# Performance work log

Measured on AMD Instinct MI355X. Metric: run time of the kernel, lower is better.

The kernel has to match this reference:

```python
import jax, jax.numpy as jnp
import numpy as np
import math

B, S, MEM, D, H = 2, 2048, 512, 1024, 16
DH = D // H  # 64


def setup_inputs() -> dict:
    key = jax.random.key(0)
    ks = jax.random.split(key, 12)
    s = 1.0 / math.sqrt(D)
    return {
        "x": jax.random.normal(ks[0], (B, S, D), jnp.float32),
        "mems": jax.random.normal(ks[1], (B, MEM, D), jnp.float32),
        "freqs_cis": jax.random.normal(ks[2], (S, 32), jnp.float32),
        "mask": jax.random.randint(ks[3], (B, MEM + S), 0, 2, jnp.int32),
        "Wq": jax.random.normal(ks[4], (D, D), jnp.float32) * s,
        "bq": jnp.zeros((D,), jnp.float32),
        "Wk": jax.random.normal(ks[5], (D, D), jnp.float32) * s,
        "bk": jnp.zeros((D,), jnp.float32),
        "Wv": jax.random.normal(ks[6], (D, D), jnp.float32) * s,
        "bv": jnp.zeros((D,), jnp.float32),
        "Wo": jax.random.normal(ks[7], (D, D), jnp.float32) * s,
        "bo": jnp.zeros((D,), jnp.float32),
    }


def _split_heads(t):
    # [B, T, D] -> [B, H, T, DH]
    b, t_, _ = t.shape
    return t.reshape(b, t_, H, DH).transpose(0, 2, 1, 3)


def reference(x, mems, freqs_cis, mask, Wq, bq, Wk, bk, Wv, bv, Wo, bo):
    # mems prepended along sequence for K/V (torch: c = cat([mems, x], 1))
    c = jnp.concatenate([mems, x], axis=1)  # [B, MEM+S, D]
    Q = _split_heads(x @ Wq.T + bq)          # [B, H, S, DH]
    K = _split_heads(c @ Wk.T + bk)          # [B, H, Skv, DH]
    V = _split_heads(c @ Wv.T + bv)          # [B, H, Skv, DH]

    scores = jnp.einsum("bhqd,bhkd->bhqk", Q, K) / math.sqrt(DH)
    m = mask.astype(jnp.float32)             # [B, Skv]
    scores = scores - 1e6 * (1.0 - m[:, None, None, :])
    attn = jax.nn.softmax(scores, axis=-1)   # dropout omitted (eval mode)
    out = jnp.einsum("bhqk,bhkd->bhqd", attn, V)  # [B, H, S, DH]
    out = out.transpose(0, 2, 1, 3).reshape(B, S, D)
    return out @ Wo.T + bo
```

## Files before the change

### kernel.cpp

```cpp
#include <hip/hip_runtime.h>
#include <math.h>

#define NB   2
#define SQ   2048
#define SMEM 512
#define SKVN 2560
#define ND   1024
#define NH   16
#define DHN  64
#define NBH  32

typedef unsigned short u16;
typedef short bf16x8 __attribute__((ext_vector_type(8)));
typedef float f32x4 __attribute__((ext_vector_type(4)));
typedef u16 u16x4 __attribute__((ext_vector_type(4)));
typedef u16 u16x8 __attribute__((ext_vector_type(8)));

#define CSC   0.1803368801111204f

__device__ __forceinline__ u16 f2bf(float f) {
    unsigned u = __float_as_uint(f);
    u += 0x7FFFu + ((u >> 16) & 1u);
    return (u16)(u >> 16);
}

__device__ __forceinline__ float bf2f(u16 v) {
    return __uint_as_float(((unsigned)v) << 16);
}

__device__ __forceinline__ void async16(u16* lds, const u16* g) {
    __builtin_amdgcn_global_load_lds(
        (const __attribute__((address_space(1))) void*)g,
        (__attribute__((address_space(3))) void*)lds, 16, 0, 0);
}

__device__ __forceinline__ unsigned lds_off(const void* p) {
    return (unsigned)(uintptr_t)(const __attribute__((address_space(3))) void*)p;
}

__device__ __forceinline__ u16x4 tr_read(unsigned a) {
    u16x4 d;
    asm volatile("ds_read_b64_tr_b16 %0, %1" : "=v"(d) : "v"(a) : "memory");
    return d;
}

__device__ __forceinline__ unsigned cvtpk(float lo, float hi) {
    unsigned r;
    asm("v_cvt_pk_bf16_f32 %0, %1, %2" : "=v"(r) : "v"(lo), "v"(hi));
    return r;
}

__device__ __forceinline__ float exp2r(float x) {
    float r;
    asm("v_exp_f32 %0, %1" : "=v"(r) : "v"(x));
    return r;
}

union PKU { unsigned u[2]; u16x4 v; };
union U8  { struct { u16x4 lo, hi; } p; bf16x8 v; };

__global__ __launch_bounds__(256)
void cvt_all(const float* __restrict__ x, const float* __restrict__ mems,
             const float* __restrict__ W0, const float* __restrict__ W1,
             const float* __restrict__ W2, const float* __restrict__ W3,
             u16* __restrict__ xb, u16* __restrict__ memb,
             u16* __restrict__ d0, u16* __restrict__ d1,
             u16* __restrict__ d2, u16* __restrict__ d3,
             const int* __restrict__ mask, u16* __restrict__ mb16)
{
    const int bid = blockIdx.x;
    if (bid >= 4608) {
        const int i = (bid - 4608) * 256 + threadIdx.x;
        if (i < NB * SKVN)
            mb16[i] = mask[i] ? (u16)0 : f2bf(1.0e6f * CSC);
        return;
    }
    size_t i = ((size_t)bid * 256 + threadIdx.x) * 8;
    const float* s; u16* d;
    if (i < 4194304) { s = x; d = xb; }
    else if (i < 5242880) { s = mems; d = memb; i -= 4194304; }
    else {
        size_t off = i - 5242880;
        const int wi = (int)(off >> 20);
        i = off & 1048575;
        switch (wi) {
            case 0:  s = W0; d = d0; break;
            case 1:  s = W1; d = d1; break;
            case 2:  s = W2; d = d2; break;
            default: s = W3; d = d3; break;
        }
    }
    float4 a = *(const float4*)(s + i);
    float4 b = *(const float4*)(s + i + 4);
    u16x8 o;
    o[0]=f2bf(a.x); o[1]=f2bf(a.y); o[2]=f2bf(a.z); o[3]=f2bf(a.w);
    o[4]=f2bf(b.x); o[5]=f2bf(b.y); o[6]=f2bf(b.z); o[7]=f2bf(b.w);
    *(u16x8*)(d + i) = o;
}

__device__ __forceinline__ const u16* arow_ptr(const u16* x, const u16* mems,
                                               int grow, int T, int memLen) {
    int b = grow >= T ? 1 : 0;
    int t = grow - b * T;
    if (memLen > 0 && t < memLen)
        return mems + ((size_t)(b * memLen + t)) * ND;
    return x + ((size_t)(b * (T - memLen) + (t - memLen))) * ND;
}

__device__ __forceinline__
void gemm_body(const u16* __restrict__ x, const u16* __restrict__ mems,
               const u16* __restrict__ W, const float* __restrict__ bias,
               void* __restrict__ out, int T, int memLen, int mode,
               int bx, int by, u16* As0, u16* As1, u16* Bs0, u16* Bs1)
{
    u16* As[2] = {As0, As1};
    u16* Bs[2] = {Bs0, Bs1};

    const int tid  = threadIdx.x;
    const int wave = tid >> 6, lane = tid & 63;
    const int lg = lane >> 4, li = lane & 15;
    const int wr = (wave >> 1) * 64, wc = (wave & 1) * 64;
    const int row0 = bx * 128, col0 = by * 128;

    const int srow = lane >> 2;
    const int sslot = lane & 3;

    f32x4 acc[4][4];
    const f32x4 zf = {0.f, 0.f, 0.f, 0.f};
#pragma unroll
    for (int m = 0; m < 4; ++m)
#pragma unroll
        for (int n = 0; n < 4; ++n) acc[m][n] = zf;

    auto stage = [&](int c, int kt) {
        const int k0 = kt * 32;
#pragma unroll
        for (int ch = wave; ch < 8; ch += 4) {
            const int r = ch * 16 + srow;
            const int gs = sslot ^ ((r ^ (r >> 2)) & 3);
            async16(&As[c][ch * 512],
                    arow_ptr(x, mems, row0 + r, T, memLen) + k0 + gs * 8);
        }
#pragma unroll
        for (int ch = wave; ch < 8; ch += 4) {
            const int r = ch * 16 + srow;
            const int gs = sslot ^ ((r ^ (r >> 2)) & 3);
            async16(&Bs[c][ch * 512],
                    W + (size_t)(col0 + r) * ND + k0 + gs * 8);
        }
    };

    stage(0, 0);
    __builtin_amdgcn_sched_barrier(0);
    stage(1, 1);
    __builtin_amdgcn_sched_barrier(0);

    int cur = 0;
    for (int kt = 0; kt < 32; ++kt) {
        if (kt == 31) asm volatile("s_waitcnt vmcnt(0)" ::: "memory");
        else          asm volatile("s_waitcnt vmcnt(4)" ::: "memory");
        __builtin_amdgcn_s_barrier();
        __builtin_amdgcn_sched_barrier(0);

        bf16x8 af[4], bfr[4];
#pragma unroll
        for (int m = 0; m < 4; ++m) {
            const int r = wr + m * 16 + li;
            af[m] = *(const bf16x8*)&As[cur][r * 32 + ((lg ^ ((r ^ (r >> 2)) & 3)) << 3)];
        }
#pragma unroll
        for (int n = 0; n < 4; ++n) {
            const int r = wc + n * 16 + li;
            bfr[n] = *(const bf16x8*)&Bs[cur][r * 32 + ((lg ^ ((r ^ (r >> 2)) & 3)) << 3)];
        }
#pragma unroll
        for (int m = 0; m < 4; ++m)
#pragma unroll
            for (int n = 0; n < 4; ++n)
                acc[m][n] = __builtin_amdgcn_mfma_f32_16x16x32_bf16(
                                af[m], bfr[n], acc[m][n], 0, 0, 0);

        asm volatile("s_waitcnt lgkmcnt(0)" ::: "memory");
        __builtin_amdgcn_s_barrier();
        __builtin_amdgcn_sched_barrier(0);

        if (kt + 2 < 32) stage(cur, kt + 2);
        cur ^= 1;
    }

#pragma unroll
    for (int n = 0; n < 4; ++n) {
        const int col = col0 + wc + n * 16 + li;
        const float bv = bias[col];
#pragma unroll
        for (int m = 0; m < 4; ++m) {
            const int rbase = row0 + wr + m * 16 + 4 * lg;
            if (mode == 1) {
                u16* o = (u16*)out;
                const int h = col >> 6, dh = col & 63;
#pragma unroll
                for (int r = 0; r < 4; ++r) {
                    const int grow = rbase + r;
                    const int b = grow >= T ? 1 : 0;
                    const int t = grow - b * T;
                    o[(((size_t)b * NH + h) * T + t) * DHN + dh] =
                        f2bf(acc[m][n][r] + bv);
                }
            } else {
                u16* o = (u16*)out;
                const int h = col >> 6, dh = col & 63;
                const int b = rbase >= T ? 1 : 0;
                const int t = rbase - b * T;
                u16x4 pk;
                pk[0] = f2bf(acc[m][n][0] + bv);
                pk[1] = f2bf(acc[m][n][1] + bv);
                pk[2] = f2bf(acc[m][n][2] + bv);
                pk[3] = f2bf(acc[m][n][3] + bv);
                *(u16x4*)&o[(((size_t)b * NH + h) * DHN + dh) * (size_t)T + t] = pk;
            }
        }
    }
}

__global__ __launch_bounds__(256)
void gemm_qkv(const u16* __restrict__ xb, const u16* __restrict__ memb,
              const u16* __restrict__ Wq, const float* __restrict__ bq, u16* Qb,
              const u16* __restrict__ Wk, const float* __restrict__ bk, u16* Kb,
              const u16* __restrict__ Wv, const float* __restrict__ bv, u16* Vtb)
{
    __shared__ u16 As[2][128 * 32];
    __shared__ u16 Bs[2][128 * 32];
    const int id = (blockIdx.x & 7) * 112 + (blockIdx.x >> 3);
    if (id < 256) {
        gemm_body(xb, nullptr, Wq, bq, Qb, SQ, 0, 1, id & 31, id >> 5,
                  As[0], As[1], Bs[0], Bs[1]);
    } else if (id < 576) {
        const int t = id - 256;
        gemm_body(xb, memb, Wk, bk, Kb, SKVN, SMEM, 1, t % 40, t / 40,
                  As[0], As[1], Bs[0], Bs[1]);
    } else {
        const int t = id - 576;
        gemm_body(xb, memb, Wv, bv, Vtb, SKVN, SMEM, 2, t % 40, t / 40,
                  As[0], As[1], Bs[0], Bs[1]);
    }
}

__global__ __launch_bounds__(256)
void gemm_o(const u16* __restrict__ x, const u16* __restrict__ W,
            const float* __restrict__ bias, float* __restrict__ out)
{
    __shared__ u16 As[2][64 * 32];
    __shared__ u16 Bs[2][128 * 32];

    const int tid  = threadIdx.x;
    const int wave = tid >> 6, lane = tid & 63;
    const int lg = lane >> 4, li = lane & 15;
    const int wr = (wave >> 1) * 32, wc = (wave & 1) * 64;

    const int id = (blockIdx.x & 7) * 64 + (blockIdx.x >> 3);
    const int row0 = (id >> 3) * 64, col0 = (id & 7) * 128;

    const int srow = lane >> 2;
    const int sslot = lane & 3;

    f32x4 acc[2][4];
    const f32x4 zf = {0.f, 0.f, 0.f, 0.f};
#pragma unroll
    for (int m = 0; m < 2; ++m)
#pragma unroll
        for (int n = 0; n < 4; ++n) acc[m][n] = zf;

    auto stage = [&](int c, int kt) {
        const int k0 = kt * 32;
        {
            const int r = wave * 16 + srow;
            const int gs = sslot ^ ((r ^ (r >> 2)) & 3);
            async16(&As[c][wave * 512],
                    x + (size_t)(row0 + r) * ND + k0 + gs * 8);
        }
#pragma unroll
        for (int ch = wave; ch < 8; ch += 4) {
            const int r = ch * 16 + srow;
            const int gs = sslot ^ ((r ^ (r >> 2)) & 3);
            async16(&Bs[c][ch * 512],
                    W + (size_t)(col0 + r) * ND + k0 + gs * 8);
        }
    };

    stage(0, 0);
    __builtin_amdgcn_sched_barrier(0);
    stage(1, 1);
    __builtin_amdgcn_sched_barrier(0);

    int cur = 0;
    for (int kt = 0; kt < 32; ++kt) {
        if (kt == 31) asm volatile("s_waitcnt vmcnt(0)" ::: "memory");
        else          asm volatile("s_waitcnt vmcnt(3)" ::: "memory");
        __builtin_amdgcn_s_barrier();
        __builtin_amdgcn_sched_barrier(0);

        bf16x8 af[2], bfr[4];
#pragma unroll
        for (int m = 0; m < 2; ++m) {
            const int r = wr + m * 16 + li;
            af[m] = *(const bf16x8*)&As[cur][r * 32 + ((lg ^ ((r ^ (r >> 2)) & 3)) << 3)];
        }
#pragma unroll
        for (int n = 0; n < 4; ++n) {
            const int r = wc + n * 16 + li;
            bfr[n] = *(const bf16x8*)&Bs[cur][r * 32 + ((lg ^ ((r ^ (r >> 2)) & 3)) << 3)];
        }
#pragma unroll
        for (int m = 0; m < 2; ++m)
#pragma unroll
            for (int n = 0; n < 4; ++n)
                acc[m][n] = __builtin_amdgcn_mfma_f32_16x16x32_bf16(
                                af[m], bfr[n], acc[m][n], 0, 0, 0);

        asm volatile("s_waitcnt lgkmcnt(0)" ::: "memory");
        __builtin_amdgcn_s_barrier();
        __builtin_amdgcn_sched_barrier(0);

        if (kt + 2 < 32) stage(cur, kt + 2);
        cur ^= 1;
    }

#pragma unroll
    for (int n = 0; n < 4; ++n) {
        const int col = col0 + wc + n * 16 + li;
        const float bv = bias[col];
#pragma unroll
        for (int m = 0; m < 2; ++m) {
            const int rbase = row0 + wr + m * 16 + 4 * lg;
#pragma unroll
            for (int r = 0; r < 4; ++r)
                out[(size_t)(rbase + r) * ND + col] = acc[m][n][r] + bv;
        }
    }
}

__global__ __launch_bounds__(512)
void attn_mfma(const u16* __restrict__ Qw, const u16* __restrict__ Kw,
               const u16* __restrict__ Vt, const u16* __restrict__ mb16,
               u16* __restrict__ AO)
{
    __shared__ u16 Ks[2][64 * 64];
    __shared__ u16 Vs[2][64 * 64];
    __shared__ u16 Ps[8][1024];
    __shared__ u16 Ms[SKVN];

    const int tid  = threadIdx.x;
    const int wave = tid >> 6, lane = tid & 63;
    const int lg = lane >> 4, li = lane & 15;

    const int wg = blockIdx.x;
    const int sw = (wg & 7) * 64 + (wg >> 3);
    const int bh = sw >> 4;
    const int q0 = (sw & 15) * 128;
    const int b = bh >> 4, h = bh & 15;

    const u16* Kg = Kw + (size_t)bh * SKVN * DHN;
    const u16* Vg = Vt + (size_t)bh * DHN * SKVN;
    const u16* m16row = mb16 + (size_t)b * SKVN;

    bf16x8 qA0, qA1;
    {
        const u16* Qp = Qw + ((size_t)bh * SQ + q0 + wave * 16 + li) * DHN;
        qA0 = *(const bf16x8*)(Qp + lg * 8);
        qA1 = *(const bf16x8*)(Qp + 32 + lg * 8);
    }

    for (int i = tid * 8; i < SKVN; i += 4096)
        *(u16x8*)&Ms[i] = *(const u16x8*)(m16row + i);

    U8 ou;
#pragma unroll
    for (int i = 0; i < 4; ++i) { ou.p.lo[i] = 0x3F80; ou.p.hi[i] = 0x3F80; }
    const bf16x8 onesb = ou.v;

    const int srow = lane >> 3, sslot = lane & 7;

    auto stage = [&](int c, int t) {
        const int kv0 = t * 64;
        const int r = wave * 8 + srow;
        async16(&Ks[c][wave * 512],
                Kg + (size_t)(kv0 + r) * DHN + ((sslot ^ (r & 7)) << 3));
        async16(&Vs[c][wave * 512],
                Vg + (size_t)r * SKVN + kv0 + ((sslot ^ (r & 7)) << 3));
    };

    f32x4 oA[4], laccA;
    const f32x4 zf = {0.f, 0.f, 0.f, 0.f};
#pragma unroll
    for (int n = 0; n < 4; ++n) oA[n] = zf;
    laccA = zf;

    u16* Pw = &Ps[wave][0];
    const unsigned paA = lds_off(Pw) + 256u * lg + 8u * li;

    __syncthreads();
    __builtin_amdgcn_sched_barrier(0);
    stage(0, 0);
    __builtin_amdgcn_sched_barrier(0);
    stage(1, 1);
    __builtin_amdgcn_sched_barrier(0);

    const int NT = SKVN / 64;
    int cur = 0;
    for (int t = 0; t < NT; ++t) {
        if (t == NT - 1) asm volatile("s_waitcnt vmcnt(0)" ::: "memory");
        else             asm volatile("s_waitcnt vmcnt(2)" ::: "memory");
        __builtin_amdgcn_s_barrier();
        __builtin_amdgcn_sched_barrier(0);

        float mbc[4];
#pragma unroll
        for (int n = 0; n < 4; ++n)
            mbc[n] = bf2f(Ms[t * 64 + n * 16 + li]);

        __builtin_amdgcn_s_setprio(1);
        f32x4 sA[4];
#pragma unroll
        for (int n = 0; n < 4; ++n) {
            const int r = n * 16 + li;
            bf16x8 kb0 = *(const bf16x8*)&Ks[cur][r * 64 + ((lg ^ (r & 7)) << 3)];
            bf16x8 kb1 = *(const bf16x8*)&Ks[cur][r * 64 + (((4 + lg) ^ (r & 7)) << 3)];
            f32x4 z = zf;
            z     = __builtin_amdgcn_mfma_f32_16x16x32_bf16(qA0, kb0, z, 0, 0, 0);
            sA[n] = __builtin_amdgcn_mfma_f32_16x16x32_bf16(qA1, kb1, z, 0, 0, 0);
        }
        __builtin_amdgcn_s_setprio(0);

#pragma unroll
        for (int n = 0; n < 4; ++n) {
            const float mb = mbc[n];
            const int pw = (n * 16 + li) * 16 + lg * 4;
            PKU ua;
            ua.u[0] = cvtpk(exp2r(fmaf(sA[n][0], CSC, -mb)),
                            exp2r(fmaf(sA[n][1], CSC, -mb)));
            ua.u[1] = cvtpk(exp2r(fmaf(sA[n][2], CSC, -mb)),
                            exp2r(fmaf(sA[n][3], CSC, -mb)));
            *(u16x4*)&Pw[pw] = ua.v;
        }

        u16x4 a00 = tr_read(paA);
        u16x4 a01 = tr_read(paA + 128);
        u16x4 a10 = tr_read(paA + 1024);
        u16x4 a11 = tr_read(paA + 1024 + 128);
        asm volatile("s_waitcnt lgkmcnt(0)" ::: "memory");
        __builtin_amdgcn_sched_barrier(0);
        U8 pA0, pA1;
        pA0.p.lo = a00; pA0.p.hi = a01;
        pA1.p.lo = a10; pA1.p.hi = a11;

        __builtin_amdgcn_s_setprio(1);
        laccA = __builtin_amdgcn_mfma_f32_16x16x32_bf16(pA0.v, onesb, laccA, 0, 0, 0);
        laccA = __builtin_amdgcn_mfma_f32_16x16x32_bf16(pA1.v, onesb, laccA, 0, 0, 0);
#pragma unroll
        for (int n = 0; n < 4; ++n) {
            const int r = n * 16 + li;
            bf16x8 vb0 = *(const bf16x8*)&Vs[cur][r * 64 + ((lg ^ (r & 7)) << 3)];
            bf16x8 vb1 = *(const bf16x8*)&Vs[cur][r * 64 + (((4 + lg) ^ (r & 7)) << 3)];
            oA[n] = __builtin_amdgcn_mfma_f32_16x16x32_bf16(pA0.v, vb0, oA[n], 0, 0, 0);
            oA[n] = __builtin_amdgcn_mfma_f32_16x16x32_bf16(pA1.v, vb1, oA[n], 0, 0, 0);
        }
        __builtin_amdgcn_s_setprio(0);

        asm volatile("s_waitcnt lgkmcnt(0)" ::: "memory");
        __builtin_amdgcn_s_barrier();
        __builtin_amdgcn_sched_barrier(0);

        if (t + 2 < NT) stage(cur, t + 2);
        cur ^= 1;
    }

#pragma unroll
    for (int r = 0; r < 4; ++r) {
        const float invA = 1.f / laccA[r];
        const int rowA = q0 + wave * 16 + 4 * lg + r;
#pragma unroll
        for (int n = 0; n < 4; ++n) {
            const int col = h * DHN + n * 16 + li;
            AO[((size_t)b * SQ + rowA) * ND + col] = f2bf(oA[n][r] * invA);
        }
    }
}

extern "C" void kernel_launch(void* const* d_in, const int* in_sizes, int n_in,
                              void* d_out, int out_size, void* d_ws, size_t ws_size,
                              hipStream_t stream)
{
    const float* x    = (const float*)d_in[0];
    const float* mems = (const float*)d_in[1];
    const int*   mask = (const int*)d_in[3];
    const float* Wq = (const float*)d_in[4];  const float* bq = (const float*)d_in[5];
    const float* Wk = (const float*)d_in[6];  const float* bk = (const float*)d_in[7];
    const float* Wv = (const float*)d_in[8];  const float* bv = (const float*)d_in[9];
    const float* Wo = (const float*)d_in[10]; const float* bo = (const float*)d_in[11];
    float* out = (float*)d_out;

    u16* ws = (u16*)d_ws;
    u16* xb   = ws;
    u16* memb = xb   + (size_t)NB * SQ * ND;
    u16* Wqb  = memb + (size_t)NB * SMEM * ND;
    u16* Wkb  = Wqb + (size_t)ND * ND;
    u16* Wvb  = Wkb + (size_t)ND * ND;
    u16* Wob  = Wvb + (size_t)ND * ND;
    u16* Qb   = Wob + (size_t)ND * ND;
    u16* Kb   = Qb  + (size_t)NB * NH * SQ * DHN;
    u16* Vtb  = Kb  + (size_t)NB * NH * SKVN * DHN;
    u16* AOb  = Vtb + (size_t)NB * NH * SKVN * DHN;
    u16* mb16 = AOb + (size_t)NB * SQ * ND;

    const dim3 blk(256);
    cvt_all<<<dim3(4628), blk, 0, stream>>>(x, mems, Wq, Wk, Wv, Wo,
                                            xb, memb, Wqb, Wkb, Wvb, Wob,
                                            mask, mb16);
    gemm_qkv<<<dim3(896), blk, 0, stream>>>(xb, memb,
                                            Wqb, bq, Qb,
                                            Wkb, bk, Kb,
                                            Wvb, bv, Vtb);
    attn_mfma<<<dim3(512), dim3(512), 0, stream>>>(Qb, Kb, Vtb, mb16, AOb);
    gemm_o<<<dim3(512), blk, 0, stream>>>(AOb, Wob, bo, out);
}
```

Measured before the change: 157.7 us.

## Switch projection GEMMs to single-wave 64x64 tiles without workgroup barriers

Replaces the 4-wave 128x128 (and 64x128) GEMM tiles with a single-wave 64x64 tile body shared by the QKV and output projections. Each wave stages its own A and B tiles into LDS, so the s_barrier calls are removed. The next-stage prefetch is now issued before the MFMA block. This cuts synchronization and raises the workgroup count, at the cost of less operand reuse per tile and more global/L2 traffic.

```diff
diff --git a/kernel.cpp b/kernel.cpp
--- a/kernel.cpp
+++ b/kernel.cpp
@@ -108,19 +108,17 @@
 }
 
 __device__ __forceinline__
-void gemm_body(const u16* __restrict__ x, const u16* __restrict__ mems,
-               const u16* __restrict__ W, const float* __restrict__ bias,
-               void* __restrict__ out, int T, int memLen, int mode,
-               int bx, int by, u16* As0, u16* As1, u16* Bs0, u16* Bs1)
+void gemm64_body(const u16* __restrict__ x, const u16* __restrict__ mems,
+                 const u16* __restrict__ W, const float* __restrict__ bias,
+                 void* __restrict__ out, int T, int memLen, int mode,
+                 int bx, int by, u16* As0, u16* As1, u16* Bs0, u16* Bs1)
 {
     u16* As[2] = {As0, As1};
     u16* Bs[2] = {Bs0, Bs1};
 
-    const int tid  = threadIdx.x;
-    const int wave = tid >> 6, lane = tid & 63;
+    const int lane = threadIdx.x;
     const int lg = lane >> 4, li = lane & 15;
-    const int wr = (wave >> 1) * 64, wc = (wave & 1) * 64;
-    const int row0 = bx * 128, col0 = by * 128;
+    const int row0 = bx * 64, col0 = by * 64;
 
     const int srow = lane >> 2;
     const int sslot = lane & 3;
@@ -135,14 +133,14 @@
     auto stage = [&](int c, int kt) {
         const int k0 = kt * 32;
 #pragma unroll
-        for (int ch = wave; ch < 8; ch += 4) {
+        for (int ch = 0; ch < 4; ++ch) {
             const int r = ch * 16 + srow;
             const int gs = sslot ^ ((r ^ (r >> 2)) & 3);
             async16(&As[c][ch * 512],
                     arow_ptr(x, mems, row0 + r, T, memLen) + k0 + gs * 8);
         }
 #pragma unroll
-        for (int ch = wave; ch < 8; ch += 4) {
+        for (int ch = 0; ch < 4; ++ch) {
             const int r = ch * 16 + srow;
             const int gs = sslot ^ ((r ^ (r >> 2)) & 3);
             async16(&Bs[c][ch * 512],
@@ -158,44 +156,46 @@
     int cur = 0;
     for (int kt = 0; kt < 32; ++kt) {
         if (kt == 31) asm volatile("s_waitcnt vmcnt(0)" ::: "memory");
-        else          asm volatile("s_waitcnt vmcnt(4)" ::: "memory");
-        __builtin_amdgcn_s_barrier();
+        else          asm volatile("s_waitcnt vmcnt(8)" ::: "memory");
         __builtin_amdgcn_sched_barrier(0);
 
         bf16x8 af[4], bfr[4];
 #pragma unroll
         for (int m = 0; m < 4; ++m) {
-            const int r = wr + m * 16 + li;
+            const int r = m * 16 + li;
             af[m] = *(const bf16x8*)&As[cur][r * 32 + ((lg ^ ((r ^ (r >> 2)) & 3)) << 3)];
         }
 #pragma unroll
         for (int n = 0; n < 4; ++n) {
-            const int r = wc + n * 16 + li;
+            const int r = n * 16 + li;
             bfr[n] = *(const bf16x8*)&Bs[cur][r * 32 + ((lg ^ ((r ^ (r >> 2)) & 3)) << 3)];
         }
+        asm volatile("s_waitcnt lgkmcnt(0)" ::: "memory");
+        __builtin_amdgcn_sched_barrier(0);
+        if (kt + 2 < 32) stage(cur, kt + 2);
+
 #pragma unroll
         for (int m = 0; m < 4; ++m)
 #pragma unroll
             for (int n = 0; n < 4; ++n)
                 acc[m][n] = __builtin_amdgcn_mfma_f32_16x16x32_bf16(
                                 af[m], bfr[n], acc[m][n], 0, 0, 0);
-
-        asm volatile("s_waitcnt lgkmcnt(0)" ::: "memory");
-        __builtin_amdgcn_s_barrier();
-        __builtin_amdgcn_sched_barrier(0);
-
-        if (kt + 2 < 32) stage(cur, kt + 2);
         cur ^= 1;
     }
 
 #pragma unroll
     for (int n = 0; n < 4; ++n) {
-        const int col = col0 + wc + n * 16 + li;
+        const int col = col0 + n * 16 + li;
         const float bv = bias[col];
 #pragma unroll
         for (int m = 0; m < 4; ++m) {
-            const int rbase = row0 + wr + m * 16 + 4 * lg;
-            if (mode == 1) {
+            const int rbase = row0 + m * 16 + 4 * lg;
+            if (mode == 0) {
+                float* o = (float*)out;
+#pragma unroll
+                for (int r = 0; r < 4; ++r)
+                    o[(size_t)(rbase + r) * ND + col] = acc[m][n][r] + bv;
+            } else if (mode == 1) {
                 u16* o = (u16*)out;
                 const int h = col >> 6, dh = col & 63;
 #pragma unroll
@@ -222,121 +222,38 @@
     }
 }
 
-__global__ __launch_bounds__(256)
+__global__ __launch_bounds__(64)
 void gemm_qkv(const u16* __restrict__ xb, const u16* __restrict__ memb,
               const u16* __restrict__ Wq, const float* __restrict__ bq, u16* Qb,
               const u16* __restrict__ Wk, const float* __restrict__ bk, u16* Kb,
               const u16* __restrict__ Wv, const float* __restrict__ bv, u16* Vtb)
 {
-    __shared__ u16 As[2][128 * 32];
-    __shared__ u16 Bs[2][128 * 32];
-    const int id = (blockIdx.x & 7) * 112 + (blockIdx.x >> 3);
-    if (id < 256) {
-        gemm_body(xb, nullptr, Wq, bq, Qb, SQ, 0, 1, id & 31, id >> 5,
-                  As[0], As[1], Bs[0], Bs[1]);
-    } else if (id < 576) {
-        const int t = id - 256;
-        gemm_body(xb, memb, Wk, bk, Kb, SKVN, SMEM, 1, t % 40, t / 40,
-                  As[0], As[1], Bs[0], Bs[1]);
+    __shared__ u16 As[2][64 * 32];
+    __shared__ u16 Bs[2][64 * 32];
+    const int id = (blockIdx.x & 7) * 448 + (blockIdx.x >> 3);
+    if (id < 1024) {
+        gemm64_body(xb, nullptr, Wq, bq, Qb, SQ, 0, 1, id >> 4, id & 15,
+                    As[0], As[1], Bs[0], Bs[1]);
+    } else if (id < 2304) {
+        const int t = id - 1024;
+        gemm64_body(xb, memb, Wk, bk, Kb, SKVN, SMEM, 1, t >> 4, t & 15,
+                    As[0], As[1], Bs[0], Bs[1]);
     } else {
-        const int t = id - 576;
-        gemm_body(xb, memb, Wv, bv, Vtb, SKVN, SMEM, 2, t % 40, t / 40,
-                  As[0], As[1], Bs[0], Bs[1]);
-    }
-}
-
-__global__ __launch_bounds__(256)
+        const int t = id - 2304;
+        gemm64_body(xb, memb, Wv, bv, Vtb, SKVN, SMEM, 2, t >> 4, t & 15,
+                    As[0], As[1], Bs[0], Bs[1]);
+    }
+}
+
+__global__ __launch_bounds__(64)
 void gemm_o(const u16* __restrict__ x, const u16* __restrict__ W,
             const float* __restrict__ bias, float* __restrict__ out)
 {
     __shared__ u16 As[2][64 * 32];
-    __shared__ u16 Bs[2][128 * 32];
-
-    const int tid  = threadIdx.x;
-    const int wave = tid >> 6, lane = tid & 63;
-    const int lg = lane >> 4, li = lane & 15;
-    const int wr = (wave >> 1) * 32, wc = (wave & 1) * 64;
-
-    const int id = (blockIdx.x & 7) * 64 + (blockIdx.x >> 3);
-    const int row0 = (id >> 3) * 64, col0 = (id & 7) * 128;
-
-    const int srow = lane >> 2;
-    const int sslot = lane & 3;
-
-    f32x4 acc[2][4];
-    const f32x4 zf = {0.f, 0.f, 0.f, 0.f};
-#pragma unroll
-    for (int m = 0; m < 2; ++m)
-#pragma unroll
-        for (int n = 0; n < 4; ++n) acc[m][n] = zf;
-
-    auto stage = [&](int c, int kt) {
-        const int k0 = kt * 32;
-        {
-            const int r = wave * 16 + srow;
-            const int gs = sslot ^ ((r ^ (r >> 2)) & 3);
-            async16(&As[c][wave * 512],
-                    x + (size_t)(row0 + r) * ND + k0 + gs * 8);
-        }
-#pragma unroll
-        for (int ch = wave; ch < 8; ch += 4) {
-            const int r = ch * 16 + srow;
-            const int gs = sslot ^ ((r ^ (r >> 2)) & 3);
-            async16(&Bs[c][ch * 512],
-                    W + (size_t)(col0 + r) * ND + k0 + gs * 8);
-        }
-    };
-
-    stage(0, 0);
-    __builtin_amdgcn_sched_barrier(0);
-    stage(1, 1);
-    __builtin_amdgcn_sched_barrier(0);
-
-    int cur = 0;
-    for (int kt = 0; kt < 32; ++kt) {
-        if (kt == 31) asm volatile("s_waitcnt vmcnt(0)" ::: "memory");
-        else          asm volatile("s_waitcnt vmcnt(3)" ::: "memory");
-        __builtin_amdgcn_s_barrier();
-        __builtin_amdgcn_sched_barrier(0);
-
-        bf16x8 af[2], bfr[4];
-#pragma unroll
-        for (int m = 0; m < 2; ++m) {
-            const int r = wr + m * 16 + li;
-            af[m] = *(const bf16x8*)&As[cur][r * 32 + ((lg ^ ((r ^ (r >> 2)) & 3)) << 3)];
-        }
-#pragma unroll
-        for (int n = 0; n < 4; ++n) {
-            const int r = wc + n * 16 + li;
-            bfr[n] = *(const bf16x8*)&Bs[cur][r * 32 + ((lg ^ ((r ^ (r >> 2)) & 3)) << 3)];
-        }
-#pragma unroll
-        for (int m = 0; m < 2; ++m)
-#pragma unroll
-            for (int n = 0; n < 4; ++n)
-                acc[m][n] = __builtin_amdgcn_mfma_f32_16x16x32_bf16(
-                                af[m], bfr[n], acc[m][n], 0, 0, 0);
-
-        asm volatile("s_waitcnt lgkmcnt(0)" ::: "memory");
-        __builtin_amdgcn_s_barrier();
-        __builtin_amdgcn_sched_barrier(0);
-
-        if (kt + 2 < 32) stage(cur, kt + 2);
-        cur ^= 1;
-    }
-
-#pragma unroll
-    for (int n = 0; n < 4; ++n) {
-        const int col = col0 + wc + n * 16 + li;
-        const float bv = bias[col];
-#pragma unroll
-        for (int m = 0; m < 2; ++m) {
-            const int rbase = row0 + wr + m * 16 + 4 * lg;
-#pragma unroll
-            for (int r = 0; r < 4; ++r)
-                out[(size_t)(rbase + r) * ND + col] = acc[m][n][r] + bv;
-        }
-    }
+    __shared__ u16 Bs[2][64 * 32];
+    const int id = (blockIdx.x & 7) * 128 + (blockIdx.x >> 3);
+    gemm64_body(x, nullptr, W, bias, out, SQ, 0, 0, id >> 4, id & 15,
+                As[0], As[1], Bs[0], Bs[1]);
 }
 
 __global__ __launch_bounds__(512)
@@ -516,10 +433,10 @@
     cvt_all<<<dim3(4628), blk, 0, stream>>>(x, mems, Wq, Wk, Wv, Wo,
                                             xb, memb, Wqb, Wkb, Wvb, Wob,
                                             mask, mb16);
-    gemm_qkv<<<dim3(896), blk, 0, stream>>>(xb, memb,
-                                            Wqb, bq, Qb,
-                                            Wkb, bk, Kb,
-                                            Wvb, bv, Vtb);
+    gemm_qkv<<<dim3(3584), dim3(64), 0, stream>>>(xb, memb,
+                                                  Wqb, bq, Qb,
+                                                  Wkb, bk, Kb,
+                                                  Wvb, bv, Vtb);
     attn_mfma<<<dim3(512), dim3(512), 0, stream>>>(Qb, Kb, Vtb, mb16, AOb);
-    gemm_o<<<dim3(512), blk, 0, stream>>>(AOb, Wob, bo, out);
-}
+    gemm_o<<<dim3(1024), dim3(64), 0, stream>>>(AOb, Wob, bo, out);
+}
```

Measured after the change: 150.1 us, median of 3. 4.8% less time.
